# Kernel tuning notes

Hardware: AMD Instinct MI355X
Metric: run time of the kernel (lower is better)

## Reference

```python
import jax, jax.numpy as jnp
import numpy as np

N = 100000   # amino-acid nodes
D = 128      # prot_hidden_dim == input_dim (output_dim)
E = 600000   # edges per relation
L = 3        # prot_num_layers
EPS = 1e-5   # BatchNorm eps


def setup_inputs() -> dict:
    key = jax.random.key(0)
    ks = jax.random.split(key, 16)
    x = jax.random.normal(ks[0], (N, D), jnp.float32)
    seq_src = jax.random.randint(ks[1], (E,), 0, N)
    seq_dst = jax.random.randint(ks[2], (E,), 0, N)
    knn_src = jax.random.randint(ks[3], (E,), 0, N)
    knn_dst = jax.random.randint(ks[4], (E,), 0, N)
    dis_src = jax.random.randint(ks[5], (E,), 0, N)
    dis_dst = jax.random.randint(ks[6], (E,), 0, N)
    # GraphConv weights/biases: [layer, relation, ...]
    Wrel = jax.random.normal(ks[7], (L, 3, D, D), jnp.float32) * (1.0 / np.sqrt(D))
    brel = jax.random.normal(ks[8], (L, 3, D), jnp.float32) * 0.02
    # per-layer fc (last maps hidden -> output_dim == D)
    Wfc = jax.random.normal(ks[9], (L, D, D), jnp.float32) * (1.0 / np.sqrt(D))
    bfc = jax.random.normal(ks[10], (L, D), jnp.float32) * 0.02
    # BatchNorm (eval mode) for layers l=0,1
    gamma = 1.0 + 0.1 * jax.random.normal(ks[11], (L - 1, D), jnp.float32)
    beta = 0.1 * jax.random.normal(ks[12], (L - 1, D), jnp.float32)
    run_mean = 0.1 * jax.random.normal(ks[13], (L - 1, D), jnp.float32)
    run_var = jax.random.uniform(ks[14], (L - 1, D), jnp.float32, 0.5, 1.5)
    return dict(x=x, seq_src=seq_src, seq_dst=seq_dst, knn_src=knn_src,
                knn_dst=knn_dst, dis_src=dis_src, dis_dst=dis_dst,
                Wrel=Wrel, brel=brel, Wfc=Wfc, bfc=bfc,
                gamma=gamma, beta=beta, run_mean=run_mean, run_var=run_var)


def _deg_norms(src, dst):
    # DGL norm='both': out-degree of src, in-degree of dst, clamped to >=1
    ones = jnp.ones(src.shape, jnp.float32)
    out_deg = jnp.clip(jax.ops.segment_sum(ones, src, num_segments=N), 1.0)
    in_deg = jnp.clip(jax.ops.segment_sum(ones, dst, num_segments=N), 1.0)
    return out_deg ** -0.5, in_deg ** -0.5


def reference(x, seq_src, seq_dst, knn_src, knn_dst, dis_src, dis_dst,
              Wrel, brel, Wfc, bfc, gamma, beta, run_mean, run_var):
    rels = [(seq_src, seq_dst), (knn_src, knn_dst), (dis_src, dis_dst)]
    norms = [_deg_norms(s, d) for s, d in rels]
    h = x
    for l in range(L):
        agg = jnp.zeros((N, D), h.dtype)
        for r, (s, d) in enumerate(rels):
            ns, nd = norms[r]
            # GraphConv norm='both', in==out feats: weight first, then propagate
            m = (h @ Wrel[l, r]) * ns[:, None]           # [N, D]
            msg = jax.ops.segment_sum(m[s], d, num_segments=N)  # gather-scatter
            agg = agg + msg * nd[:, None] + brel[l, r]
        h = agg @ Wfc[l] + bfc[l]
        if l < L - 1:
            # eval-mode BatchNorm1d + ReLU (dropout is identity in eval)
            h = (h - run_mean[l]) * jax.lax.rsqrt(run_var[l] + EPS) * gamma[l] + beta[l]
            h = jax.nn.relu(h)
    return h
```

## Files before the change

kernel.cpp:

```cpp
#include <hip/hip_runtime.h>
#include <math.h>

#define N_NODES 100000
#define D 128
#define E_EDGES 600000
#define BN_EPS 1e-5f
#define RPS (N_NODES + 4)
#define N4V (N_NODES / 4)
#define SCAN_BLOCKS ((N4V + 255) / 256)

typedef __attribute__((ext_vector_type(8))) __bf16 bf16x8;
typedef __attribute__((ext_vector_type(4))) __bf16 bf16x4;
typedef __attribute__((ext_vector_type(16))) float f32x16;

__device__ __forceinline__ int qswz(int row, int q) { return q ^ (row & 15); }
__device__ __forceinline__ int swz(int row, int c) { return c ^ ((row >> 1) & 3); }

__global__ __launch_bounds__(256) void hist_kernel(
    const int* __restrict__ s0, const int* __restrict__ d0,
    const int* __restrict__ s1, const int* __restrict__ d1,
    const int* __restrict__ s2, const int* __restrict__ d2,
    int* __restrict__ outdeg, int* __restrict__ indeg)
{
    const int r = blockIdx.y;
    const int* src = (r == 0) ? s0 : ((r == 1) ? s1 : s2);
    const int* dst = (r == 0) ? d0 : ((r == 1) ? d1 : d2);
    int* od = outdeg + (size_t)r * N_NODES;
    int* id = indeg + (size_t)r * N_NODES;
    int i4 = blockIdx.x * 256 + threadIdx.x;
    if (i4 < E_EDGES / 4) {
        int4 s = ((const int4*)src)[i4];
        int4 d = ((const int4*)dst)[i4];
        atomicAdd(&od[s.x], 1); atomicAdd(&od[s.y], 1);
        atomicAdd(&od[s.z], 1); atomicAdd(&od[s.w], 1);
        atomicAdd(&id[d.x], 1); atomicAdd(&id[d.y], 1);
        atomicAdd(&id[d.z], 1); atomicAdd(&id[d.w], 1);
    }
}

__global__ __launch_bounds__(256) void norm_kernel(
    const int* __restrict__ outdeg, const int* __restrict__ indeg,
    float* __restrict__ ns, float* __restrict__ nd)
{
    int n = blockIdx.x * 256 + threadIdx.x;
    int r = blockIdx.y;
    if (n < N_NODES) {
        int od = outdeg[r * N_NODES + n];
        int id = indeg[r * N_NODES + n];
        ns[r * N_NODES + n] = rsqrtf((float)(od < 1 ? 1 : od));
        nd[r * N_NODES + n] = rsqrtf((float)(id < 1 ? 1 : id));
    }
}

__global__ __launch_bounds__(256) void scan_part_kernel(
    const int* __restrict__ indeg, int* __restrict__ rowptr, int* __restrict__ bsum)
{
    const int r = blockIdx.y;
    const int t = threadIdx.x;
    const int lane = t & 63, wid = t >> 6;
    __shared__ int wsum[4], woff[4];
    int i4 = blockIdx.x * 256 + t;
    int4 v = (i4 < N4V) ? ((const int4*)(indeg + (size_t)r * N_NODES))[i4]
                        : make_int4(0, 0, 0, 0);
    int s0 = v.x, s1 = s0 + v.y, s2 = s1 + v.z, s3 = s2 + v.w;
    int x = s3;
    #pragma unroll
    for (int off = 1; off < 64; off <<= 1) {
        int y = __shfl_up(x, off);
        if (lane >= off) x += y;
    }
    if (lane == 63) wsum[wid] = x;
    __syncthreads();
    if (t < 4) { int s = 0; for (int j = 0; j < t; ++j) s += wsum[j]; woff[t] = s; }
    __syncthreads();
    int base = woff[wid] + (x - s3);
    if (i4 < N4V) {
        int idx = i4 * 4;
        int* rp = rowptr + (size_t)r * RPS;
        rp[idx] = base; rp[idx + 1] = base + s0; rp[idx + 2] = base + s1; rp[idx + 3] = base + s2;
    }
    if (t == 255) bsum[r * SCAN_BLOCKS + blockIdx.x] = woff[3] + wsum[3];
}

__global__ __launch_bounds__(256) void scan_mid_kernel(
    int* __restrict__ bsum, int* __restrict__ rowptr)
{
    const int t = threadIdx.x;
    const int lane = t & 63, wid = t >> 6;
    if (wid >= 3) return;
    const int r = wid;
    int carry = 0;
    for (int c = 0; c < (SCAN_BLOCKS + 63) / 64; ++c) {
        int idx = c * 64 + lane;
        int v = (idx < SCAN_BLOCKS) ? bsum[r * SCAN_BLOCKS + idx] : 0;
        int x = v;
        #pragma unroll
        for (int off = 1; off < 64; off <<= 1) {
            int y = __shfl_up(x, off);
            if (lane >= off) x += y;
        }
        if (idx < SCAN_BLOCKS) bsum[r * SCAN_BLOCKS + idx] = carry + x - v;
        carry += __shfl(x, 63);
    }
    if (lane == 0) rowptr[(size_t)r * RPS + N_NODES] = carry;
}

__global__ __launch_bounds__(256) void scan_add_kernel(
    int* __restrict__ rowptr, const int* __restrict__ bsum, int* __restrict__ cursor)
{
    const int r = blockIdx.y;
    int i4 = blockIdx.x * 256 + threadIdx.x;
    if (i4 < N4V) {
        int off = bsum[r * SCAN_BLOCKS + blockIdx.x];
        int4* rp4 = (int4*)(rowptr + (size_t)r * RPS);
        int4 v = rp4[i4];
        v.x += off; v.y += off; v.z += off; v.w += off;
        rp4[i4] = v;
        ((int4*)(cursor + (size_t)r * N_NODES))[i4] = v;
    }
}

__global__ __launch_bounds__(256) void fill_kernel(
    const int* __restrict__ s0, const int* __restrict__ d0,
    const int* __restrict__ s1, const int* __restrict__ d1,
    const int* __restrict__ s2, const int* __restrict__ d2,
    const float* __restrict__ nsv,
    int* __restrict__ cursor, int2* __restrict__ eint)
{
    const int r = blockIdx.y;
    const int* src = (r == 0) ? s0 : ((r == 1) ? s1 : s2);
    const int* dst = (r == 0) ? d0 : ((r == 1) ? d1 : d2);
    int* cur = cursor + (size_t)r * N_NODES;
    int2* eg = eint + (size_t)r * E_EDGES;
    const float* ns_ = nsv + (size_t)r * N_NODES;
    int i = blockIdx.x * 256 + threadIdx.x;
    if (i < E_EDGES) {
        int s = src[i];
        int d = dst[i];
        int pos = atomicAdd(&cur[d], 1);
        eg[pos] = make_int2(s, __float_as_int(ns_[s]));
    }
}

__global__ __launch_bounds__(256) void wprep_kernel(
    const float* __restrict__ Wrel, const float* __restrict__ Wfc,
    const float* __restrict__ gma, const float* __restrict__ rvar,
    __bf16* __restrict__ Whi, __bf16* __restrict__ Wlo)
{
    __shared__ float W2[128][132];
    __shared__ float W1p[16][132];
    const int b = blockIdx.x;
    const int l = b / 3;
    const int by = blockIdx.y;
    const int t = threadIdx.x;

    const float* src1 = Wrel + (size_t)b * D * D;
    const float* src2 = Wfc + (size_t)l * D * D;
    #pragma unroll
    for (int p = 0; p < 16; ++p) {
        int u = t + p * 256;
        int r = u >> 5, f = u & 31;
        *(float4*)&W2[r][f * 4] = *(const float4*)(src2 + r * D + f * 4);
    }
    #pragma unroll
    for (int p = 0; p < 2; ++p) {
        int u = t + p * 256;
        int r = u >> 5, f = u & 31;
        *(float4*)&W1p[r][f * 4] = *(const float4*)(src1 + (size_t)(by * 16 + r) * D + f * 4);
    }
    __syncthreads();

    const int rl = t >> 4;
    const int cb = (t & 15) * 8;
    float acc[8];
    #pragma unroll
    for (int j = 0; j < 8; ++j) acc[j] = 0.f;
    for (int k = 0; k < 128; ++k) {
        float a = W1p[rl][k];
        #pragma unroll
        for (int j = 0; j < 8; ++j) acc[j] = fmaf(a, W2[k][cb + j], acc[j]);
    }
    const int row = by * 16 + rl;
    #pragma unroll
    for (int j = 0; j < 8; ++j) {
        int colj = cb + j;
        float s = 1.0f;
        if (l < 2) s = gma[l * D + colj] * rsqrtf(rvar[l * D + colj] + BN_EPS);
        float v = acc[j] * s;
        __bf16 hb = (__bf16)v;
        __bf16 lb = (__bf16)(v - (float)hb);
        Whi[((size_t)b * D + colj) * D + row] = hb;
        Wlo[((size_t)b * D + colj) * D + row] = lb;
    }
}

__global__ __launch_bounds__(128) void bias_prep_kernel(
    const float* __restrict__ brel, const float* __restrict__ Wfc,
    const float* __restrict__ bfc,
    const float* __restrict__ gma, const float* __restrict__ bta,
    const float* __restrict__ rmean, const float* __restrict__ rvar,
    float* __restrict__ bvec)
{
    int j = threadIdx.x;
    int l = blockIdx.x;
    float acc = bfc[l * D + j];
    for (int k = 0; k < D; ++k) {
        float bs = brel[(l * 3 + 0) * D + k] + brel[(l * 3 + 1) * D + k] + brel[(l * 3 + 2) * D + k];
        acc = fmaf(bs, Wfc[((size_t)l * D + k) * D + j], acc);
    }
    if (l < 2) {
        float s = gma[l * D + j] * rsqrtf(rvar[l * D + j] + BN_EPS);
        acc = acc * s + (bta[l * D + j] - rmean[l * D + j] * s);
    }
    bvec[l * D + j] = acc;
}

#define FMA16(W_, P_, Q_, R_, S_)                                              \
    a0.x = fmaf(W_, P_.x, a0.x); a0.y = fmaf(W_, P_.y, a0.y);                  \
    a0.z = fmaf(W_, P_.z, a0.z); a0.w = fmaf(W_, P_.w, a0.w);                  \
    a1.x = fmaf(W_, Q_.x, a1.x); a1.y = fmaf(W_, Q_.y, a1.y);                  \
    a1.z = fmaf(W_, Q_.z, a1.z); a1.w = fmaf(W_, Q_.w, a1.w);                  \
    a2.x = fmaf(W_, R_.x, a2.x); a2.y = fmaf(W_, R_.y, a2.y);                  \
    a2.z = fmaf(W_, R_.z, a2.z); a2.w = fmaf(W_, R_.w, a2.w);                  \
    a3.x = fmaf(W_, S_.x, a3.x); a3.y = fmaf(W_, S_.y, a3.y);                  \
    a3.z = fmaf(W_, S_.z, a3.z); a3.w = fmaf(W_, S_.w, a3.w);

__global__ __launch_bounds__(512, 4) void fused_layer_kernel(
    const float* __restrict__ h,
    const int* __restrict__ rowptr,
    const int2* __restrict__ eint,
    const float* __restrict__ ndv,
    const __bf16* __restrict__ Whi,
    const __bf16* __restrict__ Wlo,
    float* __restrict__ out, const float* __restrict__ bias, int relu)
{
    __shared__ __bf16 Ah[128 * 128];
    __shared__ __bf16 Al[128 * 128];
    __shared__ __bf16 Bh[128 * 32];
    __shared__ __bf16 Bl[128 * 32];

    const int t = threadIdx.x;
    const int lane = t & 63;
    const int wid = t >> 6;
    const int wrow = wid & 3;
    const int wcol = wid >> 2;
    const int row0 = blockIdx.x * 128;
    const int g = t >> 3;
    const int gl = t & 7;

    f32x16 acc[2];
    #pragma unroll
    for (int nt = 0; nt < 2; ++nt)
        #pragma unroll
        for (int i = 0; i < 16; ++i) acc[nt][i] = 0.0f;

    for (int r = 0; r < 3; ++r) {
        const int* rp = rowptr + (size_t)r * RPS;
        const int2* eg = eint + (size_t)r * E_EDGES;
        const float* nd_ = ndv + (size_t)r * N_NODES;

        #pragma unroll
        for (int rr = 0; rr < 2; ++rr) {
            int rowl = g * 2 + rr;
            int grow = row0 + rowl;
            float4 a0 = {0,0,0,0}, a1 = {0,0,0,0}, a2 = {0,0,0,0}, a3 = {0,0,0,0};
            if (grow < N_NODES) {
                int beg = rp[grow], end = rp[grow + 1];
                float sc = nd_[grow];
                int e = beg;
                for (; e + 4 <= end; e += 4) {
                    int2 q0 = eg[e], q1 = eg[e + 1], q2 = eg[e + 2], q3 = eg[e + 3];
                    const float* p0 = h + (size_t)q0.x * D + gl * 4;
                    const float* p1 = h + (size_t)q1.x * D + gl * 4;
                    const float* p2 = h + (size_t)q2.x * D + gl * 4;
                    const float* p3 = h + (size_t)q3.x * D + gl * 4;
                    float4 u00 = *(const float4*)(p0),      u01 = *(const float4*)(p0 + 32);
                    float4 u02 = *(const float4*)(p0 + 64), u03 = *(const float4*)(p0 + 96);
                    float4 u10 = *(const float4*)(p1),      u11 = *(const float4*)(p1 + 32);
                    float4 u12 = *(const float4*)(p1 + 64), u13 = *(const float4*)(p1 + 96);
                    float4 u20 = *(const float4*)(p2),      u21 = *(const float4*)(p2 + 32);
                    float4 u22 = *(const float4*)(p2 + 64), u23 = *(const float4*)(p2 + 96);
                    float4 u30 = *(const float4*)(p3),      u31 = *(const float4*)(p3 + 32);
                    float4 u32 = *(const float4*)(p3 + 64), u33 = *(const float4*)(p3 + 96);
                    float wa = __int_as_float(q0.y), wb = __int_as_float(q1.y);
                    float wc = __int_as_float(q2.y), wd = __int_as_float(q3.y);
                    FMA16(wa, u00, u01, u02, u03);
                    FMA16(wb, u10, u11, u12, u13);
                    FMA16(wc, u20, u21, u22, u23);
                    FMA16(wd, u30, u31, u32, u33);
                }
                if (e + 2 <= end) {
                    int2 q0 = eg[e], q1 = eg[e + 1];
                    const float* p0 = h + (size_t)q0.x * D + gl * 4;
                    const float* p1 = h + (size_t)q1.x * D + gl * 4;
                    float4 u00 = *(const float4*)(p0),      u01 = *(const float4*)(p0 + 32);
                    float4 u02 = *(const float4*)(p0 + 64), u03 = *(const float4*)(p0 + 96);
                    float4 u10 = *(const float4*)(p1),      u11 = *(const float4*)(p1 + 32);
                    float4 u12 = *(const float4*)(p1 + 64), u13 = *(const float4*)(p1 + 96);
                    float wa = __int_as_float(q0.y), wb = __int_as_float(q1.y);
                    FMA16(wa, u00, u01, u02, u03);
                    FMA16(wb, u10, u11, u12, u13);
                    e += 2;
                }
                if (e < end) {
                    int2 q0 = eg[e];
                    const float* p0 = h + (size_t)q0.x * D + gl * 4;
                    float4 u00 = *(const float4*)(p0),      u01 = *(const float4*)(p0 + 32);
                    float4 u02 = *(const float4*)(p0 + 64), u03 = *(const float4*)(p0 + 96);
                    float wa = __int_as_float(q0.y);
                    FMA16(wa, u00, u01, u02, u03);
                }
                a0.x *= sc; a0.y *= sc; a0.z *= sc; a0.w *= sc;
                a1.x *= sc; a1.y *= sc; a1.z *= sc; a1.w *= sc;
                a2.x *= sc; a2.y *= sc; a2.z *= sc; a2.w *= sc;
                a3.x *= sc; a3.y *= sc; a3.z *= sc; a3.w *= sc;
            }
            float4 av[4] = {a0, a1, a2, a3};
            #pragma unroll
            for (int j = 0; j < 4; ++j) {
                int q = (gl >> 1) + 4 * j;
                int idx = rowl * 128 + qswz(rowl, q) * 8 + (gl & 1) * 4;
                bf16x4 hv, lv;
                float* ap = &av[j].x;
                #pragma unroll
                for (int c = 0; c < 4; ++c) {
                    __bf16 hb = (__bf16)ap[c];
                    hv[c] = hb;
                    lv[c] = (__bf16)(ap[c] - (float)hb);
                }
                *(bf16x4*)&Ah[idx] = hv;
                *(bf16x4*)&Al[idx] = lv;
            }
        }

        for (int ks = 0; ks < 4; ++ks) {
            {
                int colj = t >> 2;
                int c = t & 3;
                int idx = colj * 32 + swz(colj, c) * 8;
                const __bf16* sh = Whi + (size_t)r * D * D + (size_t)colj * D + ks * 32 + c * 8;
                const __bf16* sl = Wlo + (size_t)r * D * D + (size_t)colj * D + ks * 32 + c * 8;
                *(bf16x8*)&Bh[idx] = *(const bf16x8*)sh;
                *(bf16x8*)&Bl[idx] = *(const bf16x8*)sl;
            }
            __syncthreads();

            const int arow = lane & 31;
            const int kgrp = lane >> 5;
            #pragma unroll
            for (int ksub = 0; ksub < 2; ++ksub) {
                int ac = ksub * 2 + kgrp;
                int arow_g = wrow * 32 + arow;
                int aidx = arow_g * 128 + qswz(arow_g, ks * 4 + ac) * 8;
                bf16x8 ahv = *(const bf16x8*)&Ah[aidx];
                bf16x8 alv = *(const bf16x8*)&Al[aidx];
                #pragma unroll
                for (int nt = 0; nt < 2; ++nt) {
                    int colg = wcol * 64 + nt * 32 + arow;
                    int bidx = colg * 32 + swz(colg, ac) * 8;
                    bf16x8 bhv = *(const bf16x8*)&Bh[bidx];
                    bf16x8 blv = *(const bf16x8*)&Bl[bidx];
                    acc[nt] = __builtin_amdgcn_mfma_f32_32x32x16_bf16(ahv, bhv, acc[nt], 0, 0, 0);
                    acc[nt] = __builtin_amdgcn_mfma_f32_32x32x16_bf16(ahv, blv, acc[nt], 0, 0, 0);
                    acc[nt] = __builtin_amdgcn_mfma_f32_32x32x16_bf16(alv, bhv, acc[nt], 0, 0, 0);
                }
            }
            __syncthreads();
        }
    }

    const int colb = lane & 31;
    const int rq = lane >> 5;
    #pragma unroll
    for (int nt = 0; nt < 2; ++nt) {
        int colg = wcol * 64 + nt * 32 + colb;
        float bv = bias[colg];
        #pragma unroll
        for (int reg = 0; reg < 16; ++reg) {
            int rowl = wrow * 32 + (reg & 3) + 8 * (reg >> 2) + 4 * rq;
            int grow = row0 + rowl;
            if (grow < N_NODES) {
                float z = acc[nt][reg] + bv;
                if (relu) z = fmaxf(z, 0.f);
                out[(size_t)grow * D + colg] = z;
            }
        }
    }
}

extern "C" void kernel_launch(void* const* d_in, const int* in_sizes, int n_in,
                              void* d_out, int out_size, void* d_ws, size_t ws_size,
                              hipStream_t stream)
{
    const float* x      = (const float*)d_in[0];
    const int* seq_src  = (const int*)d_in[1];
    const int* seq_dst  = (const int*)d_in[2];
    const int* knn_src  = (const int*)d_in[3];
    const int* knn_dst  = (const int*)d_in[4];
    const int* dis_src  = (const int*)d_in[5];
    const int* dis_dst  = (const int*)d_in[6];
    const float* Wrel   = (const float*)d_in[7];
    const float* brel   = (const float*)d_in[8];
    const float* Wfc    = (const float*)d_in[9];
    const float* bfc    = (const float*)d_in[10];
    const float* gma    = (const float*)d_in[11];
    const float* bta    = (const float*)d_in[12];
    const float* rmean  = (const float*)d_in[13];
    const float* rvar   = (const float*)d_in[14];
    float* out = (float*)d_out;

    const size_t ND = (size_t)N_NODES * D;
    float* ws   = (float*)d_ws;
    float* h0   = ws;
    float* h1   = h0 + ND;
    float* ns_  = h1 + ND;
    float* nd_  = ns_ + 3 * N_NODES;
    float* bvec = nd_ + 3 * N_NODES;
    __bf16* Whi = (__bf16*)(bvec + 3 * D);
    __bf16* Wlo = Whi + (size_t)9 * D * D;
    int* outdeg = (int*)(Wlo + (size_t)9 * D * D);
    int* indeg  = outdeg + 3 * N_NODES;
    int* rowptr = indeg + 3 * N_NODES;
    int* cursor = rowptr + 3 * RPS;
    int* bsum   = cursor + 3 * N_NODES;
    int2* eint  = (int2*)(bsum + 3 * SCAN_BLOCKS + 2);

    hipMemsetAsync(outdeg, 0, (size_t)6 * N_NODES * sizeof(int), stream);
    hist_kernel<<<dim3((E_EDGES / 4 + 255) / 256, 3), 256, 0, stream>>>(
        seq_src, seq_dst, knn_src, knn_dst, dis_src, dis_dst, outdeg, indeg);
    norm_kernel<<<dim3((N_NODES + 255) / 256, 3), 256, 0, stream>>>(outdeg, indeg, ns_, nd_);
    scan_part_kernel<<<dim3(SCAN_BLOCKS, 3), 256, 0, stream>>>(indeg, rowptr, bsum);
    scan_mid_kernel<<<1, 256, 0, stream>>>(bsum, rowptr);
    scan_add_kernel<<<dim3(SCAN_BLOCKS, 3), 256, 0, stream>>>(rowptr, bsum, cursor);
    fill_kernel<<<dim3((E_EDGES + 255) / 256, 3), 256, 0, stream>>>(
        seq_src, seq_dst, knn_src, knn_dst, dis_src, dis_dst, ns_, cursor, eint);

    wprep_kernel<<<dim3(9, 8), 256, 0, stream>>>(Wrel, Wfc, gma, rvar, Whi, Wlo);
    bias_prep_kernel<<<3, 128, 0, stream>>>(brel, Wfc, bfc, gma, bta, rmean, rvar, bvec);

    const int GB = (N_NODES + 127) / 128;
    fused_layer_kernel<<<GB, 512, 0, stream>>>(
        x, rowptr, eint, nd_, Whi, Wlo, h0, bvec, 1);
    fused_layer_kernel<<<GB, 512, 0, stream>>>(
        h0, rowptr, eint, nd_, Whi + (size_t)3 * D * D, Wlo + (size_t)3 * D * D,
        h1, bvec + D, 1);
    fused_layer_kernel<<<GB, 512, 0, stream>>>(
        h1, rowptr, eint, nd_, Whi + (size_t)6 * D * D, Wlo + (size_t)6 * D * D,
        out, bvec + 2 * D, 0);
}
```

Baseline: 787.3 us.

## Halve fused layer tile to 64 rows, read weights from global, fold norm kernel

The fused gather+GEMM kernel now processes 64 rows per block instead of 128. Each thread gathers one row instead of two, and each wave computes a single 32x32 output tile. The B-operand weights are read straight from global/L2 instead of being staged through shared memory, which drops the per-k-step barriers and cuts LDS use so more blocks can be resident (launch bounds go to 8 blocks per SM). The degree-normalisation kernel is folded into scan_add to save a launch. The cost is more weight reloads from cache per output and twice as many blocks.

```diff
diff --git a/kernel.cpp b/kernel.cpp
--- a/kernel.cpp
+++ b/kernel.cpp
@@ -14,7 +14,6 @@
 typedef __attribute__((ext_vector_type(16))) float f32x16;
 
 __device__ __forceinline__ int qswz(int row, int q) { return q ^ (row & 15); }
-__device__ __forceinline__ int swz(int row, int c) { return c ^ ((row >> 1) & 3); }
 
 __global__ __launch_bounds__(256) void hist_kernel(
     const int* __restrict__ s0, const int* __restrict__ d0,
@@ -35,20 +34,6 @@
         atomicAdd(&od[s.z], 1); atomicAdd(&od[s.w], 1);
         atomicAdd(&id[d.x], 1); atomicAdd(&id[d.y], 1);
         atomicAdd(&id[d.z], 1); atomicAdd(&id[d.w], 1);
-    }
-}
-
-__global__ __launch_bounds__(256) void norm_kernel(
-    const int* __restrict__ outdeg, const int* __restrict__ indeg,
-    float* __restrict__ ns, float* __restrict__ nd)
-{
-    int n = blockIdx.x * 256 + threadIdx.x;
-    int r = blockIdx.y;
-    if (n < N_NODES) {
-        int od = outdeg[r * N_NODES + n];
-        int id = indeg[r * N_NODES + n];
-        ns[r * N_NODES + n] = rsqrtf((float)(od < 1 ? 1 : od));
-        nd[r * N_NODES + n] = rsqrtf((float)(id < 1 ? 1 : id));
     }
 }
 
@@ -106,7 +91,9 @@
 }
 
 __global__ __launch_bounds__(256) void scan_add_kernel(
-    int* __restrict__ rowptr, const int* __restrict__ bsum, int* __restrict__ cursor)
+    int* __restrict__ rowptr, const int* __restrict__ bsum, int* __restrict__ cursor,
+    const int* __restrict__ outdeg, const int* __restrict__ indeg,
+    float* __restrict__ ns, float* __restrict__ nd)
 {
     const int r = blockIdx.y;
     int i4 = blockIdx.x * 256 + threadIdx.x;
@@ -117,6 +104,19 @@
         v.x += off; v.y += off; v.z += off; v.w += off;
         rp4[i4] = v;
         ((int4*)(cursor + (size_t)r * N_NODES))[i4] = v;
+        int4 od = ((const int4*)(outdeg + (size_t)r * N_NODES))[i4];
+        int4 id = ((const int4*)(indeg + (size_t)r * N_NODES))[i4];
+        float4 nsv, ndv;
+        nsv.x = rsqrtf((float)(od.x < 1 ? 1 : od.x));
+        nsv.y = rsqrtf((float)(od.y < 1 ? 1 : od.y));
+        nsv.z = rsqrtf((float)(od.z < 1 ? 1 : od.z));
+        nsv.w = rsqrtf((float)(od.w < 1 ? 1 : od.w));
+        ndv.x = rsqrtf((float)(id.x < 1 ? 1 : id.x));
+        ndv.y = rsqrtf((float)(id.y < 1 ? 1 : id.y));
+        ndv.z = rsqrtf((float)(id.z < 1 ? 1 : id.z));
+        ndv.w = rsqrtf((float)(id.w < 1 ? 1 : id.w));
+        ((float4*)(ns + (size_t)r * N_NODES))[i4] = nsv;
+        ((float4*)(nd + (size_t)r * N_NODES))[i4] = ndv;
     }
 }
 
@@ -225,7 +225,7 @@
     a3.x = fmaf(W_, S_.x, a3.x); a3.y = fmaf(W_, S_.y, a3.y);                  \
     a3.z = fmaf(W_, S_.z, a3.z); a3.w = fmaf(W_, S_.w, a3.w);
 
-__global__ __launch_bounds__(512, 4) void fused_layer_kernel(
+__global__ __launch_bounds__(512, 8) void fused_layer_kernel(
     const float* __restrict__ h,
     const int* __restrict__ rowptr,
     const int2* __restrict__ eint,
@@ -234,34 +234,33 @@
     const __bf16* __restrict__ Wlo,
     float* __restrict__ out, const float* __restrict__ bias, int relu)
 {
-    __shared__ __bf16 Ah[128 * 128];
-    __shared__ __bf16 Al[128 * 128];
-    __shared__ __bf16 Bh[128 * 32];
-    __shared__ __bf16 Bl[128 * 32];
+    __shared__ __bf16 Ah[64 * 128];
+    __shared__ __bf16 Al[64 * 128];
 
     const int t = threadIdx.x;
     const int lane = t & 63;
     const int wid = t >> 6;
-    const int wrow = wid & 3;
-    const int wcol = wid >> 2;
-    const int row0 = blockIdx.x * 128;
+    const int wrow = wid & 1;
+    const int wcol = wid >> 1;
+    const int row0 = blockIdx.x * 64;
     const int g = t >> 3;
     const int gl = t & 7;
 
-    f32x16 acc[2];
-    #pragma unroll
-    for (int nt = 0; nt < 2; ++nt)
-        #pragma unroll
-        for (int i = 0; i < 16; ++i) acc[nt][i] = 0.0f;
+    f32x16 acc;
+    #pragma unroll
+    for (int i = 0; i < 16; ++i) acc[i] = 0.0f;
+
+    const int arow = lane & 31;
+    const int kgrp = lane >> 5;
+    const int colg = wcol * 32 + arow;
 
     for (int r = 0; r < 3; ++r) {
         const int* rp = rowptr + (size_t)r * RPS;
         const int2* eg = eint + (size_t)r * E_EDGES;
         const float* nd_ = ndv + (size_t)r * N_NODES;
 
-        #pragma unroll
-        for (int rr = 0; rr < 2; ++rr) {
-            int rowl = g * 2 + rr;
+        {
+            int rowl = g;
             int grow = row0 + rowl;
             float4 a0 = {0,0,0,0}, a1 = {0,0,0,0}, a2 = {0,0,0,0}, a3 = {0,0,0,0};
             if (grow < N_NODES) {
@@ -332,57 +331,42 @@
                 *(bf16x4*)&Al[idx] = lv;
             }
         }
-
+        __syncthreads();
+
+        const __bf16* bh_base = Whi + (size_t)r * D * D + (size_t)colg * D;
+        const __bf16* bl_base = Wlo + (size_t)r * D * D + (size_t)colg * D;
+        #pragma unroll
         for (int ks = 0; ks < 4; ++ks) {
-            {
-                int colj = t >> 2;
-                int c = t & 3;
-                int idx = colj * 32 + swz(colj, c) * 8;
-                const __bf16* sh = Whi + (size_t)r * D * D + (size_t)colj * D + ks * 32 + c * 8;
-                const __bf16* sl = Wlo + (size_t)r * D * D + (size_t)colj * D + ks * 32 + c * 8;
-                *(bf16x8*)&Bh[idx] = *(const bf16x8*)sh;
-                *(bf16x8*)&Bl[idx] = *(const bf16x8*)sl;
-            }
-            __syncthreads();
-
-            const int arow = lane & 31;
-            const int kgrp = lane >> 5;
             #pragma unroll
             for (int ksub = 0; ksub < 2; ++ksub) {
                 int ac = ksub * 2 + kgrp;
+                bf16x8 bhv = *(const bf16x8*)(bh_base + ks * 32 + ac * 8);
+                bf16x8 blv = *(const bf16x8*)(bl_base + ks * 32 + ac * 8);
                 int arow_g = wrow * 32 + arow;
                 int aidx = arow_g * 128 + qswz(arow_g, ks * 4 + ac) * 8;
                 bf16x8 ahv = *(const bf16x8*)&Ah[aidx];
                 bf16x8 alv = *(const bf16x8*)&Al[aidx];
-                #pragma unroll
-                for (int nt = 0; nt < 2; ++nt) {
-                    int colg = wcol * 64 + nt * 32 + arow;
-                    int bidx = colg * 32 + swz(colg, ac) * 8;
-                    bf16x8 bhv = *(const bf16x8*)&Bh[bidx];
-                    bf16x8 blv = *(const bf16x8*)&Bl[bidx];
-                    acc[nt] = __builtin_amdgcn_mfma_f32_32x32x16_bf16(ahv, bhv, acc[nt], 0, 0, 0);
-                    acc[nt] = __builtin_amdgcn_mfma_f32_32x32x16_bf16(ahv, blv, acc[nt], 0, 0, 0);
-                    acc[nt] = __builtin_amdgcn_mfma_f32_32x32x16_bf16(alv, bhv, acc[nt], 0, 0, 0);
-                }
+                acc = __builtin_amdgcn_mfma_f32_32x32x16_bf16(ahv, bhv, acc, 0, 0, 0);
+                acc = __builtin_amdgcn_mfma_f32_32x32x16_bf16(ahv, blv, acc, 0, 0, 0);
+                acc = __builtin_amdgcn_mfma_f32_32x32x16_bf16(alv, bhv, acc, 0, 0, 0);
             }
-            __syncthreads();
         }
+        __syncthreads();
     }
 
     const int colb = lane & 31;
     const int rq = lane >> 5;
-    #pragma unroll
-    for (int nt = 0; nt < 2; ++nt) {
-        int colg = wcol * 64 + nt * 32 + colb;
-        float bv = bias[colg];
+    {
+        int colgo = wcol * 32 + colb;
+        float bv = bias[colgo];
         #pragma unroll
         for (int reg = 0; reg < 16; ++reg) {
             int rowl = wrow * 32 + (reg & 3) + 8 * (reg >> 2) + 4 * rq;
             int grow = row0 + rowl;
             if (grow < N_NODES) {
-                float z = acc[nt][reg] + bv;
+                float z = acc[reg] + bv;
                 if (relu) z = fmaxf(z, 0.f);
-                out[(size_t)grow * D + colg] = z;
+                out[(size_t)grow * D + colgo] = z;
             }
         }
     }
@@ -428,17 +412,17 @@
     hipMemsetAsync(outdeg, 0, (size_t)6 * N_NODES * sizeof(int), stream);
     hist_kernel<<<dim3((E_EDGES / 4 + 255) / 256, 3), 256, 0, stream>>>(
         seq_src, seq_dst, knn_src, knn_dst, dis_src, dis_dst, outdeg, indeg);
-    norm_kernel<<<dim3((N_NODES + 255) / 256, 3), 256, 0, stream>>>(outdeg, indeg, ns_, nd_);
     scan_part_kernel<<<dim3(SCAN_BLOCKS, 3), 256, 0, stream>>>(indeg, rowptr, bsum);
     scan_mid_kernel<<<1, 256, 0, stream>>>(bsum, rowptr);
-    scan_add_kernel<<<dim3(SCAN_BLOCKS, 3), 256, 0, stream>>>(rowptr, bsum, cursor);
+    scan_add_kernel<<<dim3(SCAN_BLOCKS, 3), 256, 0, stream>>>(
+        rowptr, bsum, cursor, outdeg, indeg, ns_, nd_);
     fill_kernel<<<dim3((E_EDGES + 255) / 256, 3), 256, 0, stream>>>(
         seq_src, seq_dst, knn_src, knn_dst, dis_src, dis_dst, ns_, cursor, eint);
 
     wprep_kernel<<<dim3(9, 8), 256, 0, stream>>>(Wrel, Wfc, gma, rvar, Whi, Wlo);
     bias_prep_kernel<<<3, 128, 0, stream>>>(brel, Wfc, bfc, gma, bta, rmean, rvar, bvec);
 
-    const int GB = (N_NODES + 127) / 128;
+    const int GB = (N_NODES + 63) / 64;
     fused_layer_kernel<<<GB, 512, 0, stream>>>(
         x, rowptr, eint, nd_, Whi, Wlo, h0, bvec, 1);
     fused_layer_kernel<<<GB, 512, 0, stream>>>(
```

New measurement: 1.094 ms. 38.9% more time.
